# Kernel tuning notes

Hardware: AMD Instinct MI355X
Metric: run time of the kernel (lower is better)

The kernel has to match this reference:

```python
import jax, jax.numpy as jnp
import numpy as np

H = 1024  # hidden_size
O = 768   # output_size == g_bert_emb_dim
B = 256   # batch
T = 256   # tgt_len
SRC_LEN = 2


def setup_inputs() -> dict:
    key = jax.random.key(0)
    ks = jax.random.split(key, 9)
    s = 1.0 / np.sqrt(H)
    return {
        "src": jax.random.normal(ks[0], (SRC_LEN, B, O), jnp.float32),
        "tgt": jax.random.randint(ks[1], (T, B), 0, 30000),
        "hidden": jax.random.normal(ks[2], (1, B, H), jnp.float32),
        # PyTorch nn.GRU params, gate order (r, z, n)
        "w_ih": jax.random.uniform(ks[3], (3 * H, O), jnp.float32, -s, s),
        "w_hh": jax.random.uniform(ks[4], (3 * H, H), jnp.float32, -s, s),
        "b_ih": jax.random.uniform(ks[5], (3 * H,), jnp.float32, -s, s),
        "b_hh": jax.random.uniform(ks[6], (3 * H,), jnp.float32, -s, s),
        # nn.Linear(hidden_size, output_size)
        "w_fc": jax.random.uniform(ks[7], (O, H), jnp.float32, -s, s),
        "b_fc": jax.random.uniform(ks[8], (O,), jnp.float32, -s, s),
    }


def reference(src, tgt, hidden, w_ih, w_hh, b_ih, b_hh, w_fc, b_fc):
    tgt_len = tgt.shape[0]

    def step(carry, _):
        x, h = carry  # x: [B, O] (previous fc output), h: [B, H]
        gi = x @ w_ih.T + b_ih          # [B, 3H]
        gh = h @ w_hh.T + b_hh          # [B, 3H]
        i_r, i_z, i_n = jnp.split(gi, 3, axis=-1)
        h_r, h_z, h_n = jnp.split(gh, 3, axis=-1)
        r = jax.nn.sigmoid(i_r + h_r)
        z = jax.nn.sigmoid(i_z + h_z)
        n = jnp.tanh(i_n + r * h_n)
        h_new = (1.0 - z) * n + z * h
        y = h_new @ w_fc.T + b_fc       # fc feedback, [B, O]
        return (y, h_new), y

    x0 = src[0]          # [B, O]
    h0 = hidden[0]       # [B, H] (num_layers = 1)
    _, outputs = jax.lax.scan(step, (x0, h0), None, length=tgt_len)
    return outputs  # [T, B, O]
```

## Files before the change

kernel.cpp:

```cpp
#include <hip/hip_runtime.h>
#include <stdint.h>

#define HDIM 1024
#define ODIM 768
#define BDIM 256
#define TLEN 256
#define G3 (3*HDIM)

typedef __attribute__((ext_vector_type(4))) float f32x4;
typedef __attribute__((ext_vector_type(8))) short s16x8;
typedef __attribute__((ext_vector_type(2))) unsigned long long u64x2;

#define SENT64 0xFFFFFFFFFFFFFFFFull

static __device__ __forceinline__ unsigned short f2bf(float f) {
  uint32_t u = __builtin_bit_cast(uint32_t, f);
  return (unsigned short)((u + 0x7fffu + ((u >> 16) & 1u)) >> 16);
}


__global__ void k_f32_to_bf16(const float* __restrict__ in, unsigned short* __restrict__ out, int n4) {
  int i = blockIdx.x * 256 + threadIdx.x;
  if (i >= n4) return;
  float4 v = ((const float4*)in)[i];
  ushort4 o;
  o.x = f2bf(v.x); o.y = f2bf(v.y); o.z = f2bf(v.z); o.w = f2bf(v.w);
  ((ushort4*)out)[i] = o;
}

__global__ void k_transpose_f32_bf16(const float* __restrict__ in, unsigned short* __restrict__ out, int R, int C) {
  __shared__ float tile[32][33];
  int c0 = blockIdx.x * 32, r0 = blockIdx.y * 32;
  int tx = threadIdx.x, ty = threadIdx.y;
  #pragma unroll
  for (int i = 0; i < 32; i += 8)
    tile[ty + i][tx] = in[(size_t)(r0 + ty + i) * C + (c0 + tx)];
  __syncthreads();
  #pragma unroll
  for (int i = 0; i < 32; i += 8)
    out[(size_t)(c0 + ty + i) * R + (r0 + tx)] = f2bf(tile[tx][ty + i]);
}

__global__ void k_bcomb(const float* __restrict__ w_ih, const float* __restrict__ b_ih,
                        const float* __restrict__ b_fc, float* __restrict__ bc) {
  int gw = (blockIdx.x * 256 + threadIdx.x) >> 6;
  int lane = threadIdx.x & 63;
  if (gw >= G3) return;
  const float* row = w_ih + (size_t)gw * ODIM;
  float s = 0.f;
  for (int o = lane; o < ODIM; o += 64) s += row[o] * b_fc[o];
  #pragma unroll
  for (int off = 32; off; off >>= 1) s += __shfl_down(s, off);
  if (lane == 0) bc[gw] = s + b_ih[gw];
}

template<bool OUT_BF16, bool ADD_BIAS>
__global__ __launch_bounds__(256) void k_gemm_bt(
    const unsigned short* __restrict__ A,
    const unsigned short* __restrict__ Bm,
    const float* __restrict__ bias,
    void* __restrict__ Cout,
    int M, int N, int K)
{
  __shared__ f32x4 red[4][32][64];
  int m0 = blockIdx.x * 64, n0 = blockIdx.y * 128;
  int w = threadIdx.x >> 6, lane = threadIdx.x & 63;
  int c = lane & 15, klane = (lane >> 4) << 3;
  int kpw = K >> 2, kw0 = w * kpw;
  f32x4 acc[4][8];
  #pragma unroll
  for (int mf = 0; mf < 4; mf++)
    #pragma unroll
    for (int nf = 0; nf < 8; nf++) acc[mf][nf] = f32x4{0.f, 0.f, 0.f, 0.f};

  for (int kk = 0; kk < kpw; kk += 32) {
    int kb = kw0 + kk + klane;
    s16x8 a[4], b[8];
    #pragma unroll
    for (int mf = 0; mf < 4; mf++)
      a[mf] = *(const s16x8*)(A + (size_t)(m0 + mf*16 + c) * K + kb);
    #pragma unroll
    for (int nf = 0; nf < 8; nf++)
      b[nf] = *(const s16x8*)(Bm + (size_t)(n0 + nf*16 + c) * K + kb);
    #pragma unroll
    for (int mf = 0; mf < 4; mf++)
      #pragma unroll
      for (int nf = 0; nf < 8; nf++)
        acc[mf][nf] = __builtin_amdgcn_mfma_f32_16x16x32_bf16(a[mf], b[nf], acc[mf][nf], 0, 0, 0);
  }
  #pragma unroll
  for (int mf = 0; mf < 4; mf++)
    #pragma unroll
    for (int nf = 0; nf < 8; nf++)
      red[w][mf*8+nf][lane] = acc[mf][nf];
  __syncthreads();
  #pragma unroll
  for (int nf = 0; nf < 8; nf++) {
    f32x4 s = red[0][w*8+nf][lane];
    #pragma unroll
    for (int w2 = 1; w2 < 4; w2++) s += red[w2][w*8+nf][lane];
    int col = n0 + nf*16 + c;
    float bv = 0.f;
    if constexpr (ADD_BIAS) bv = bias[col];
    int rb = m0 + w*16 + ((lane >> 4) << 2);
    #pragma unroll
    for (int i = 0; i < 4; i++) {
      float val = s[i] + bv;
      if constexpr (OUT_BF16)
        ((unsigned short*)Cout)[(size_t)(rb + i) * N + col] = f2bf(val);
      else
        ((float*)Cout)[(size_t)(rb + i) * N + col] = val;
    }
  }
}

__global__ __launch_bounds__(256) void k_gemm_hseq(
    const unsigned long long* __restrict__ Ahx,
    const unsigned short* __restrict__ Bm,
    const float* __restrict__ bias,
    float* __restrict__ Cout)
{
  const int M = TLEN*BDIM, N = ODIM, K = HDIM;
  __shared__ f32x4 red[4][32][64];
  int m0 = blockIdx.x * 64, n0 = blockIdx.y * 128;
  int w = threadIdx.x >> 6, lane = threadIdx.x & 63;
  int c = lane & 15, klane = (lane >> 4) << 3;
  int kpw = K >> 2, kw0 = w * kpw;
  const int tb = m0 >> 8, mgb = (m0 >> 6) & 3;
  f32x4 acc[4][8];
  #pragma unroll
  for (int mf = 0; mf < 4; mf++)
    #pragma unroll
    for (int nf = 0; nf < 8; nf++) acc[mf][nf] = f32x4{0.f, 0.f, 0.f, 0.f};

  for (int kk = 0; kk < kpw; kk += 32) {
    int kb = kw0 + kk + klane;
    int uk = kb >> 2;
    s16x8 a[4], b[8];
    #pragma unroll
    for (int mf = 0; mf < 4; mf++)
      a[mf] = *(const s16x8*)(Ahx + (((size_t)((tb*64 + (uk>>2))*4 + mgb)) << 8)
                                   + (size_t)(mf*16 + c)*4 + (uk & 3));
    #pragma unroll
    for (int nf = 0; nf < 8; nf++)
      b[nf] = *(const s16x8*)(Bm + (size_t)(n0 + nf*16 + c) * K + kb);
    #pragma unroll
    for (int mf = 0; mf < 4; mf++)
      #pragma unroll
      for (int nf = 0; nf < 8; nf++)
        acc[mf][nf] = __builtin_amdgcn_mfma_f32_16x16x32_bf16(a[mf], b[nf], acc[mf][nf], 0, 0, 0);
  }
  #pragma unroll
  for (int mf = 0; mf < 4; mf++)
    #pragma unroll
    for (int nf = 0; nf < 8; nf++)
      red[w][mf*8+nf][lane] = acc[mf][nf];
  __syncthreads();
  #pragma unroll
  for (int nf = 0; nf < 8; nf++) {
    f32x4 s = red[0][w*8+nf][lane];
    #pragma unroll
    for (int w2 = 1; w2 < 4; w2++) s += red[w2][w*8+nf][lane];
    int col = n0 + nf*16 + c;
    float bv = bias[col];
    int rb = m0 + w*16 + ((lane >> 4) << 2);
    #pragma unroll
    for (int i = 0; i < 4; i++)
      Cout[(size_t)(rb + i) * N + col] = s[i] + bv;
  }
}

__global__ __launch_bounds__(256, 1) void k_gru_persist(
    const unsigned short* __restrict__ h0b,
    const unsigned short* __restrict__ wcomb,
    const unsigned short* __restrict__ whh,
    const float* __restrict__ bcomb,
    const float* __restrict__ bhh,
    const float* __restrict__ gi0,
    const float* __restrict__ hidden0,
    unsigned long long* __restrict__ hx64)
{
  __shared__ f32x4 red[4][24][64];
  __shared__ unsigned long long tile64[64][4];
  unsigned short* tile = (unsigned short*)tile64;

  const int wg = blockIdx.x;
  const int mg = wg & 3, p = wg >> 2;
  const int tid = threadIdx.x;
  const int w = tid >> 6, lane = tid & 63;
  const int c = lane & 15, klane = (lane >> 4) << 3, rq = (lane >> 4) << 2;
  const int u0 = p * 16, u = u0 + c, m0 = mg * 64;
  const int wk0 = w * 256;
  const int rp = lane >> 5;
  const int q0 = ((lane >> 4) & 1) << 1;
  const int cprod = 16 * w + (lane & 15);

  const float bcr = bcomb[u], bcz = bcomb[HDIM + u], bcn = bcomb[2*HDIM + u];
  const float bhr = bhh[u],   bhz = bhh[HDIM + u],   bhn = bhh[2*HDIM + u];

  s16x8 wr[6][8];
  #pragma unroll
  for (int g = 0; g < 6; g++) {
    const unsigned short* W = (g < 3) ? (wcomb + (size_t)g * HDIM * HDIM)
                                      : (whh   + (size_t)(g - 3) * HDIM * HDIM);
    const unsigned short* Wrow = W + (size_t)(u0 + c) * HDIM + wk0 + klane;
    #pragma unroll
    for (int ks = 0; ks < 8; ks++)
      wr[g][ks] = *(const s16x8*)(Wrow + ks * 32);
  }

  float hcar[4];

  #pragma unroll 1
  for (int t = 0; t < TLEN; t++) {
    s16x8 a[8][4];
    if (t == 0) {
      #pragma unroll
      for (int ks = 0; ks < 8; ks++)
        #pragma unroll
        for (int mf = 0; mf < 4; mf++)
          a[ks][mf] = *(const s16x8*)(h0b + (size_t)(m0 + mf*16 + c) * HDIM + wk0 + ks*32 + klane);
    } else {
      unsigned long long* hxp = hx64 + (size_t)(t - 1) * (64*4*256);
      {
        const unsigned long long* cn = hxp + (((size_t)(cprod*4 + mg)) << 8) + 255;
        for (;;) {
          unsigned long long v = __hip_atomic_load(cn, __ATOMIC_RELAXED, __HIP_MEMORY_SCOPE_AGENT);
          if (__all(v != SENT64)) break;
          __builtin_amdgcn_s_sleep(1);
        }
      }
      u64x2 va[8][4];
      #pragma unroll
      for (int ks = 0; ks < 8; ks++)
        #pragma unroll
        for (int mf = 0; mf < 4; mf++)
          va[ks][mf] = *(const u64x2*)(hxp + (((size_t)((16*w + 2*ks + rp)*4 + mg)) << 8)
                                            + (size_t)(mf*16 + c)*4 + q0);
      unsigned int bad = 0;
      #pragma unroll
      for (int ks = 0; ks < 8; ks++)
        #pragma unroll
        for (int mf = 0; mf < 4; mf++)
          bad |= (unsigned int)(va[ks][mf][0] == SENT64) | (unsigned int)(va[ks][mf][1] == SENT64);
      if (__any((int)bad)) {
        #pragma unroll
        for (int ks = 0; ks < 8; ks++)
          #pragma unroll
          for (int mf = 0; mf < 4; mf++) {
            unsigned long long* pb = hxp + (((size_t)((16*w + 2*ks + rp)*4 + mg)) << 8)
                                         + (size_t)(mf*16 + c)*4 + q0;
            #pragma unroll
            for (int hh = 0; hh < 2; hh++) {
              if (va[ks][mf][hh] == SENT64) {
                unsigned long long v;
                do {
                  v = __hip_atomic_load(pb + hh, __ATOMIC_RELAXED, __HIP_MEMORY_SCOPE_AGENT);
                } while (v == SENT64);
                pb[hh] = v;
                va[ks][mf][hh] = v;
              }
            }
          }
      }
      #pragma unroll
      for (int ks = 0; ks < 8; ks++)
        #pragma unroll
        for (int mf = 0; mf < 4; mf++)
          a[ks][mf] = __builtin_bit_cast(s16x8, va[ks][mf]);
    }

    f32x4 acc[4][6];
    #pragma unroll
    for (int mf = 0; mf < 4; mf++)
      #pragma unroll
      for (int g = 0; g < 6; g++) acc[mf][g] = f32x4{0.f, 0.f, 0.f, 0.f};
    #pragma unroll
    for (int ks = 0; ks < 8; ks++)
      #pragma unroll
      for (int g = 0; g < 6; g++)
        #pragma unroll
        for (int mf = 0; mf < 4; mf++)
          acc[mf][g] = __builtin_amdgcn_mfma_f32_16x16x32_bf16(a[ks][mf], wr[g][ks], acc[mf][g], 0, 0, 0);

    #pragma unroll
    for (int mf = 0; mf < 4; mf++) {
      if (mf != w) {
        #pragma unroll
        for (int g = 0; g < 6; g++) red[w][mf*6 + g][lane] = acc[mf][g];
      }
    }
    f32x4 s[6];
    #pragma unroll
    for (int mf = 0; mf < 4; mf++) {
      if (mf == w) {
        #pragma unroll
        for (int g = 0; g < 6; g++) s[g] = acc[mf][g];
      }
    }
    __syncthreads();
    #pragma unroll
    for (int w2 = 0; w2 < 4; w2++) {
      if (w2 != w) {
        #pragma unroll
        for (int g = 0; g < 6; g++) s[g] += red[w2][w*6 + g][lane];
      }
    }
    __syncthreads();

    const int rbl = w*16 + rq;
    #pragma unroll
    for (int i = 0; i < 4; i++) {
      int r = m0 + rbl + i;
      float gir, giz, gin;
      if (t == 0) {
        gir = gi0[(size_t)r * G3 + u];
        giz = gi0[(size_t)r * G3 + HDIM + u];
        gin = gi0[(size_t)r * G3 + 2*HDIM + u];
        hcar[i] = hidden0[(size_t)r * HDIM + u];
      } else {
        gir = s[0][i] + bcr; giz = s[1][i] + bcz; gin = s[2][i] + bcn;
      }
      float ghr = s[3][i] + bhr, ghz = s[4][i] + bhz, ghn = s[5][i] + bhn;
      float rg = 1.f / (1.f + __expf(-(gir + ghr)));
      float zg = 1.f / (1.f + __expf(-(giz + ghz)));
      float pn = gin + rg * ghn;
      pn = fminf(fmaxf(pn, -15.f), 15.f);
      float e2 = __expf(2.f * pn);
      float ng = (e2 - 1.f) / (e2 + 1.f);
      float hv = (1.f - zg) * ng + zg * hcar[i];
      hcar[i] = hv;
      tile[(rbl + i) * 16 + c] = f2bf(hv);
    }

    {
      unsigned long long v = tile64[tid >> 2][tid & 3];
      unsigned long long* dst = hx64 + (size_t)t * (64*4*256)
                              + (((size_t)(p*4 + mg)) << 8) + tid;
      __hip_atomic_store(dst, v, __ATOMIC_RELAXED, __HIP_MEMORY_SCOPE_AGENT);
    }
  }
}

__global__ __launch_bounds__(256) void k_gru_step(
    const unsigned short* __restrict__ A1, int K1,
    const unsigned short* __restrict__ W1,
    const float* __restrict__ b1,
    const unsigned short* __restrict__ A2,
    const unsigned short* __restrict__ W2,
    const float* __restrict__ b2,
    const float* __restrict__ hprev,
    float* __restrict__ hout,
    unsigned short* __restrict__ hseq,
    int fused)
{
  __shared__ f32x4 red[4][24][64];
  int ublk = blockIdx.x & 63, mg = blockIdx.x >> 6;
  int u0 = ublk * 16, m0 = mg * 64;
  int w = threadIdx.x >> 6, lane = threadIdx.x & 63;
  int c = lane & 15, klane = (lane >> 4) << 3;
  f32x4 acc[6][4];
  #pragma unroll
  for (int g = 0; g < 6; g++)
    #pragma unroll
    for (int mf = 0; mf < 4; mf++) acc[g][mf] = f32x4{0.f, 0.f, 0.f, 0.f};

  if (fused) {
    const int kpw = HDIM >> 2;
    int kw0 = w * kpw;
    for (int kk = 0; kk < kpw; kk += 32) {
      int kb = kw0 + kk + klane;
      s16x8 a[4], bg[6];
      #pragma unroll
      for (int mf = 0; mf < 4; mf++)
        a[mf] = *(const s16x8*)(A2 + (size_t)(m0 + mf*16 + c) * HDIM + kb);
      #pragma unroll
      for (int g = 0; g < 3; g++) {
        bg[g]   = *(const s16x8*)(W1 + (size_t)(g*HDIM + u0 + c) * HDIM + kb);
        bg[g+3] = *(const s16x8*)(W2 + (size_t)(g*HDIM + u0 + c) * HDIM + kb);
      }
      #pragma unroll
      for (int g = 0; g < 6; g++)
        #pragma unroll
        for (int mf = 0; mf < 4; mf++)
          acc[g][mf] = __builtin_amdgcn_mfma_f32_16x16x32_bf16(a[mf], bg[g], acc[g][mf], 0, 0, 0);
    }
  } else {
    {
      int kpw = K1 >> 2, kw0 = w * kpw;
      for (int kk = 0; kk < kpw; kk += 32) {
        int kb = kw0 + kk + klane;
        s16x8 a[4], bg[3];
        #pragma unroll
        for (int mf = 0; mf < 4; mf++)
          a[mf] = *(const s16x8*)(A1 + (size_t)(m0 + mf*16 + c) * K1 + kb);
        #pragma unroll
        for (int g = 0; g < 3; g++)
          bg[g] = *(const s16x8*)(W1 + (size_t)(g*HDIM + u0 + c) * K1 + kb);
        #pragma unroll
        for (int g = 0; g < 3; g++)
          #pragma unroll
          for (int mf = 0; mf < 4; mf++)
            acc[g][mf] = __builtin_amdgcn_mfma_f32_16x16x32_bf16(a[mf], bg[g], acc[g][mf], 0, 0, 0);
      }
    }
    {
      int kpw = HDIM >> 2, kw0 = w * kpw;
      for (int kk = 0; kk < kpw; kk += 32) {
        int kb = kw0 + kk + klane;
        s16x8 a[4], bg[3];
        #pragma unroll
        for (int mf = 0; mf < 4; mf++)
          a[mf] = *(const s16x8*)(A2 + (size_t)(m0 + mf*16 + c) * HDIM + kb);
        #pragma unroll
        for (int g = 0; g < 3; g++)
          bg[g] = *(const s16x8*)(W2 + (size_t)(g*HDIM + u0 + c) * HDIM + kb);
        #pragma unroll
        for (int g = 0; g < 3; g++)
          #pragma unroll
          for (int mf = 0; mf < 4; mf++)
            acc[g+3][mf] = __builtin_amdgcn_mfma_f32_16x16x32_bf16(a[mf], bg[g], acc[g+3][mf], 0, 0, 0);
      }
    }
  }

  #pragma unroll
  for (int g = 0; g < 6; g++)
    #pragma unroll
    for (int mf = 0; mf < 4; mf++)
      red[w][g*4+mf][lane] = acc[g][mf];
  __syncthreads();

  f32x4 gg[6];
  #pragma unroll
  for (int g = 0; g < 6; g++) {
    f32x4 sum = red[0][g*4+w][lane];
    #pragma unroll
    for (int w2 = 1; w2 < 4; w2++) sum += red[w2][g*4+w][lane];
    gg[g] = sum;
  }
  int u = u0 + c;
  float b1r = b1[u], b1z = b1[HDIM+u], b1n = b1[2*HDIM+u];
  float b2r = b2[u], b2z = b2[HDIM+u], b2n = b2[2*HDIM+u];
  int rb = m0 + w*16 + ((lane >> 4) << 2);
  #pragma unroll
  for (int i = 0; i < 4; i++) {
    float pre_r = gg[0][i] + b1r + gg[3][i] + b2r;
    float pre_z = gg[1][i] + b1z + gg[4][i] + b2z;
    float ghn  = gg[5][i] + b2n;
    float r = 1.f / (1.f + __expf(-pre_r));
    float z = 1.f / (1.f + __expf(-pre_z));
    float pn = gg[2][i] + b1n + r * ghn;
    pn = fminf(fmaxf(pn, -15.f), 15.f);
    float e2 = __expf(2.f * pn);
    float n = (e2 - 1.f) / (e2 + 1.f);
    size_t idx = (size_t)(rb + i) * HDIM + u;
    float hp = hprev[idx];
    float hn = (1.f - z) * n + z * hp;
    hout[idx] = hn;
    hseq[idx] = f2bf(hn);
  }
}


extern "C" void kernel_launch(void* const* d_in, const int* in_sizes, int n_in,
                              void* d_out, int out_size, void* d_ws, size_t ws_size,
                              hipStream_t stream) {
  const float* src    = (const float*)d_in[0];
  const float* hidden = (const float*)d_in[2];
  const float* w_ih   = (const float*)d_in[3];
  const float* w_hh   = (const float*)d_in[4];
  const float* b_ih   = (const float*)d_in[5];
  const float* b_hh   = (const float*)d_in[6];
  const float* w_fc   = (const float*)d_in[7];
  const float* b_fc   = (const float*)d_in[8];
  float* out = (float*)d_out;

  uint8_t* ws = (uint8_t*)d_ws;
  size_t off = 0;
  auto alloc = [&](size_t bytes) -> void* {
    void* pp = ws + off;
    off += (bytes + 255) & ~(size_t)255;
    return pp;
  };
  unsigned short* wih_b  = (unsigned short*)alloc((size_t)G3*ODIM*2);
  unsigned short* whh_b  = (unsigned short*)alloc((size_t)G3*HDIM*2);
  unsigned short* wfc_b  = (unsigned short*)alloc((size_t)ODIM*HDIM*2);
  unsigned short* wfcT_b = (unsigned short*)alloc((size_t)HDIM*ODIM*2);
  unsigned short* wcomb  = (unsigned short*)alloc((size_t)G3*HDIM*2);
  unsigned short* src0_b = (unsigned short*)alloc((size_t)BDIM*ODIM*2);
  unsigned short* h0_b   = (unsigned short*)alloc((size_t)BDIM*HDIM*2);
  float* bcomb = (float*)alloc((size_t)G3*4);
  float* hbuf0 = (float*)alloc((size_t)BDIM*HDIM*4);
  float* hbuf1 = (float*)alloc((size_t)BDIM*HDIM*4);
  unsigned short* hpp = (unsigned short*)alloc((size_t)2*BDIM*HDIM*2);
  unsigned short* hseq = (unsigned short*)alloc((size_t)TLEN*BDIM*HDIM*2);
  float* gi0 = (float*)alloc((size_t)BDIM*G3*4);
  bool big = (off <= ws_size);

  k_f32_to_bf16<<<G3*ODIM/4/256, 256, 0, stream>>>(w_ih, wih_b, G3*ODIM/4);
  k_f32_to_bf16<<<G3*HDIM/4/256, 256, 0, stream>>>(w_hh, whh_b, G3*HDIM/4);
  k_f32_to_bf16<<<ODIM*HDIM/4/256, 256, 0, stream>>>(w_fc, wfc_b, ODIM*HDIM/4);
  k_f32_to_bf16<<<BDIM*ODIM/4/256, 256, 0, stream>>>(src, src0_b, BDIM*ODIM/4);
  k_f32_to_bf16<<<BDIM*HDIM/4/256, 256, 0, stream>>>(hidden, h0_b, BDIM*HDIM/4);
  k_transpose_f32_bf16<<<dim3(HDIM/32, ODIM/32), dim3(32, 8), 0, stream>>>(w_fc, wfcT_b, ODIM, HDIM);
  k_gemm_bt<true, false><<<dim3(G3/64, HDIM/128), 256, 0, stream>>>(wih_b, wfcT_b, nullptr, wcomb, G3, HDIM, ODIM);
  k_bcomb<<<G3/4, 256, 0, stream>>>(w_ih, b_ih, b_fc, bcomb);

  if (big) {
    hipMemsetAsync(hseq, 0xFF, (size_t)TLEN*BDIM*HDIM*2, stream);
    k_gemm_bt<false, true><<<dim3(BDIM/64, G3/128), 256, 0, stream>>>(
        src0_b, wih_b, b_ih, gi0, BDIM, G3, ODIM);
    k_gru_persist<<<256, 256, 0, stream>>>(h0_b, wcomb, whh_b, bcomb, b_hh,
                                           gi0, hidden,
                                           (unsigned long long*)hseq);
    k_gemm_hseq<<<dim3(TLEN*BDIM/64, ODIM/128), 256, 0, stream>>>(
        (const unsigned long long*)hseq, wfc_b, b_fc, out);
  } else {
    for (int t = 0; t < TLEN; t++) {
      const unsigned short* aprev = (t == 0) ? h0_b : hpp + (size_t)((t-1)&1)*BDIM*HDIM;
      unsigned short* hs_cur = hpp + (size_t)(t&1)*BDIM*HDIM;
      const float* hprev_f = (t == 0) ? hidden : ((t & 1) ? hbuf0 : hbuf1);
      float* hout_f = (t & 1) ? hbuf1 : hbuf0;
      if (t == 0) {
        k_gru_step<<<256, 256, 0, stream>>>(src0_b, ODIM, wih_b, b_ih,
            aprev, whh_b, b_hh, hprev_f, hout_f, hs_cur, 0);
      } else {
        k_gru_step<<<256, 256, 0, stream>>>(aprev, HDIM, wcomb, bcomb,
            aprev, whh_b, b_hh, hprev_f, hout_f, hs_cur, 1);
      }
      k_gemm_bt<false, true><<<dim3(BDIM/64, ODIM/128), 256, 0, stream>>>(
          hs_cur, wfc_b, b_fc, out + (size_t)t*BDIM*ODIM, BDIM, ODIM, HDIM);
    }
  }
}
```

Measured before the change: 2.209 ms.

## Split persistent GRU gate GEMMs across two wave groups with 512 threads

The persistent GRU kernel now runs 512 threads per block. Waves 0-3 compute the three input-side gates from wcomb and waves 4-7 compute the three hidden-side gates from whh, so each wave holds half the weight registers and issues half the MFMAs per step. The per-step hidden-state fragments are loaded and MFMA'd in two halves to limit live registers. Shared-memory reductions are split into two buffers, and the output tile row stride is padded to avoid bank conflicts. In exchange, both wave groups read the same hidden-state fragments, and only half the waves do the elementwise gate math and stores.

```diff
diff --git a/kernel.cpp b/kernel.cpp
--- a/kernel.cpp
+++ b/kernel.cpp
@@ -120,7 +120,7 @@
     const float* __restrict__ bias,
     float* __restrict__ Cout)
 {
-  const int M = TLEN*BDIM, N = ODIM, K = HDIM;
+  const int N = ODIM, K = HDIM;
   __shared__ f32x4 red[4][32][64];
   int m0 = blockIdx.x * 64, n0 = blockIdx.y * 128;
   int w = threadIdx.x >> 6, lane = threadIdx.x & 63;
@@ -170,7 +170,7 @@
   }
 }
 
-__global__ __launch_bounds__(256, 1) void k_gru_persist(
+__global__ __launch_bounds__(512) void k_gru_persist(
     const unsigned short* __restrict__ h0b,
     const unsigned short* __restrict__ wcomb,
     const unsigned short* __restrict__ whh,
@@ -180,30 +180,31 @@
     const float* __restrict__ hidden0,
     unsigned long long* __restrict__ hx64)
 {
-  __shared__ f32x4 red[4][24][64];
-  __shared__ unsigned long long tile64[64][4];
+  __shared__ f32x4 redA[4][12][64];
+  __shared__ f32x4 redB[4][12][64];
+  __shared__ unsigned long long tile64[64][5];
   unsigned short* tile = (unsigned short*)tile64;
 
   const int wg = blockIdx.x;
   const int mg = wg & 3, p = wg >> 2;
   const int tid = threadIdx.x;
-  const int w = tid >> 6, lane = tid & 63;
+  const int wv = tid >> 6, lane = tid & 63;
+  const int kw = wv & 3, gg = wv >> 2;
   const int c = lane & 15, klane = (lane >> 4) << 3, rq = (lane >> 4) << 2;
   const int u0 = p * 16, u = u0 + c, m0 = mg * 64;
-  const int wk0 = w * 256;
+  const int wk0 = kw * 256;
   const int rp = lane >> 5;
   const int q0 = ((lane >> 4) & 1) << 1;
-  const int cprod = 16 * w + (lane & 15);
+  const int cprod = 16 * kw + (lane & 15);
 
   const float bcr = bcomb[u], bcz = bcomb[HDIM + u], bcn = bcomb[2*HDIM + u];
   const float bhr = bhh[u],   bhz = bhh[HDIM + u],   bhn = bhh[2*HDIM + u];
 
-  s16x8 wr[6][8];
-  #pragma unroll
-  for (int g = 0; g < 6; g++) {
-    const unsigned short* W = (g < 3) ? (wcomb + (size_t)g * HDIM * HDIM)
-                                      : (whh   + (size_t)(g - 3) * HDIM * HDIM);
-    const unsigned short* Wrow = W + (size_t)(u0 + c) * HDIM + wk0 + klane;
+  const unsigned short* Wbase = gg ? whh : wcomb;
+  s16x8 wr[3][8];
+  #pragma unroll
+  for (int g = 0; g < 3; g++) {
+    const unsigned short* Wrow = Wbase + (size_t)(g * HDIM + u0 + c) * HDIM + wk0 + klane;
     #pragma unroll
     for (int ks = 0; ks < 8; ks++)
       wr[g][ks] = *(const s16x8*)(Wrow + ks * 32);
@@ -213,13 +214,30 @@
 
   #pragma unroll 1
   for (int t = 0; t < TLEN; t++) {
-    s16x8 a[8][4];
+    f32x4 acc[4][3];
+    #pragma unroll
+    for (int mf = 0; mf < 4; mf++)
+      #pragma unroll
+      for (int g = 0; g < 3; g++) acc[mf][g] = f32x4{0.f, 0.f, 0.f, 0.f};
+
     if (t == 0) {
       #pragma unroll
-      for (int ks = 0; ks < 8; ks++)
-        #pragma unroll
-        for (int mf = 0; mf < 4; mf++)
-          a[ks][mf] = *(const s16x8*)(h0b + (size_t)(m0 + mf*16 + c) * HDIM + wk0 + ks*32 + klane);
+      for (int pp = 0; pp < 2; pp++) {
+        s16x8 a[4][4];
+        #pragma unroll
+        for (int ks = 0; ks < 4; ks++)
+          #pragma unroll
+          for (int mf = 0; mf < 4; mf++)
+            a[ks][mf] = *(const s16x8*)(h0b + (size_t)(m0 + mf*16 + c) * HDIM
+                                             + wk0 + (pp*4 + ks)*32 + klane);
+        #pragma unroll
+        for (int ks = 0; ks < 4; ks++)
+          #pragma unroll
+          for (int g = 0; g < 3; g++)
+            #pragma unroll
+            for (int mf = 0; mf < 4; mf++)
+              acc[mf][g] = __builtin_amdgcn_mfma_f32_16x16x32_bf16(a[ks][mf], wr[g][ks? (pp*4+ks) : pp*4], acc[mf][g], 0, 0, 0);
+      }
     } else {
       unsigned long long* hxp = hx64 + (size_t)(t - 1) * (64*4*256);
       {
@@ -230,114 +248,123 @@
           __builtin_amdgcn_s_sleep(1);
         }
       }
-      u64x2 va[8][4];
-      #pragma unroll
-      for (int ks = 0; ks < 8; ks++)
-        #pragma unroll
-        for (int mf = 0; mf < 4; mf++)
-          va[ks][mf] = *(const u64x2*)(hxp + (((size_t)((16*w + 2*ks + rp)*4 + mg)) << 8)
-                                            + (size_t)(mf*16 + c)*4 + q0);
-      unsigned int bad = 0;
-      #pragma unroll
-      for (int ks = 0; ks < 8; ks++)
-        #pragma unroll
-        for (int mf = 0; mf < 4; mf++)
-          bad |= (unsigned int)(va[ks][mf][0] == SENT64) | (unsigned int)(va[ks][mf][1] == SENT64);
-      if (__any((int)bad)) {
-        #pragma unroll
-        for (int ks = 0; ks < 8; ks++)
-          #pragma unroll
-          for (int mf = 0; mf < 4; mf++) {
-            unsigned long long* pb = hxp + (((size_t)((16*w + 2*ks + rp)*4 + mg)) << 8)
-                                         + (size_t)(mf*16 + c)*4 + q0;
+      #pragma unroll
+      for (int pp = 0; pp < 2; pp++) {
+        u64x2 va[4][4];
+        #pragma unroll
+        for (int ks = 0; ks < 4; ks++)
+          #pragma unroll
+          for (int mf = 0; mf < 4; mf++)
+            va[ks][mf] = *(const u64x2*)(hxp
+                + (((size_t)((16*kw + 2*(pp*4 + ks) + rp)*4 + mg)) << 8)
+                + (size_t)(mf*16 + c)*4 + q0);
+        unsigned int bad = 0;
+        #pragma unroll
+        for (int ks = 0; ks < 4; ks++)
+          #pragma unroll
+          for (int mf = 0; mf < 4; mf++)
+            bad |= (unsigned int)(va[ks][mf][0] == SENT64) | (unsigned int)(va[ks][mf][1] == SENT64);
+        if (__any((int)bad)) {
+          #pragma unroll
+          for (int ks = 0; ks < 4; ks++)
             #pragma unroll
-            for (int hh = 0; hh < 2; hh++) {
-              if (va[ks][mf][hh] == SENT64) {
-                unsigned long long v;
-                do {
-                  v = __hip_atomic_load(pb + hh, __ATOMIC_RELAXED, __HIP_MEMORY_SCOPE_AGENT);
-                } while (v == SENT64);
-                pb[hh] = v;
-                va[ks][mf][hh] = v;
+            for (int mf = 0; mf < 4; mf++) {
+              unsigned long long* pb = hxp
+                  + (((size_t)((16*kw + 2*(pp*4 + ks) + rp)*4 + mg)) << 8)
+                  + (size_t)(mf*16 + c)*4 + q0;
+              #pragma unroll
+              for (int hh = 0; hh < 2; hh++) {
+                if (va[ks][mf][hh] == SENT64) {
+                  unsigned long long v;
+                  do {
+                    v = __hip_atomic_load(pb + hh, __ATOMIC_RELAXED, __HIP_MEMORY_SCOPE_AGENT);
+                  } while (v == SENT64);
+                  pb[hh] = v;
+                  va[ks][mf][hh] = v;
+                }
               }
             }
-          }
-      }
-      #pragma unroll
-      for (int ks = 0; ks < 8; ks++)
-        #pragma unroll
-        for (int mf = 0; mf < 4; mf++)
-          a[ks][mf] = __builtin_bit_cast(s16x8, va[ks][mf]);
-    }
-
-    f32x4 acc[4][6];
-    #pragma unroll
-    for (int mf = 0; mf < 4; mf++)
-      #pragma unroll
-      for (int g = 0; g < 6; g++) acc[mf][g] = f32x4{0.f, 0.f, 0.f, 0.f};
-    #pragma unroll
-    for (int ks = 0; ks < 8; ks++)
-      #pragma unroll
-      for (int g = 0; g < 6; g++)
-        #pragma unroll
-        for (int mf = 0; mf < 4; mf++)
-          acc[mf][g] = __builtin_amdgcn_mfma_f32_16x16x32_bf16(a[ks][mf], wr[g][ks], acc[mf][g], 0, 0, 0);
-
-    #pragma unroll
-    for (int mf = 0; mf < 4; mf++) {
-      if (mf != w) {
-        #pragma unroll
-        for (int g = 0; g < 6; g++) red[w][mf*6 + g][lane] = acc[mf][g];
-      }
-    }
-    f32x4 s[6];
-    #pragma unroll
-    for (int mf = 0; mf < 4; mf++) {
-      if (mf == w) {
-        #pragma unroll
-        for (int g = 0; g < 6; g++) s[g] = acc[mf][g];
-      }
+        }
+        #pragma unroll
+        for (int ks = 0; ks < 4; ks++)
+          #pragma unroll
+          for (int g = 0; g < 3; g++)
+            #pragma unroll
+            for (int mf = 0; mf < 4; mf++)
+              acc[mf][g] = __builtin_amdgcn_mfma_f32_16x16x32_bf16(
+                  __builtin_bit_cast(s16x8, va[ks][mf]), wr[g][pp*4 + ks], acc[mf][g], 0, 0, 0);
+      }
+    }
+
+    f32x4 sc[3], sh[3];
+    if (gg == 0) {
+      #pragma unroll
+      for (int mf = 0; mf < 4; mf++) {
+        if (mf != kw) {
+          #pragma unroll
+          for (int g = 0; g < 3; g++) redA[kw][mf*3 + g][lane] = acc[mf][g];
+        } else {
+          #pragma unroll
+          for (int g = 0; g < 3; g++) sc[g] = acc[mf][g];
+        }
+      }
+    } else {
+      #pragma unroll
+      for (int mf = 0; mf < 4; mf++)
+        #pragma unroll
+        for (int g = 0; g < 3; g++) redB[kw][mf*3 + g][lane] = acc[mf][g];
     }
     __syncthreads();
-    #pragma unroll
-    for (int w2 = 0; w2 < 4; w2++) {
-      if (w2 != w) {
-        #pragma unroll
-        for (int g = 0; g < 6; g++) s[g] += red[w2][w*6 + g][lane];
-      }
+    if (gg == 0) {
+      #pragma unroll
+      for (int k2 = 0; k2 < 4; k2++) {
+        if (k2 != kw) {
+          #pragma unroll
+          for (int g = 0; g < 3; g++) sc[g] += redA[k2][kw*3 + g][lane];
+        }
+      }
+      #pragma unroll
+      for (int g = 0; g < 3; g++) sh[g] = redB[0][kw*3 + g][lane];
+      #pragma unroll
+      for (int k2 = 1; k2 < 4; k2++)
+        #pragma unroll
+        for (int g = 0; g < 3; g++) sh[g] += redB[k2][kw*3 + g][lane];
     }
     __syncthreads();
 
-    const int rbl = w*16 + rq;
-    #pragma unroll
-    for (int i = 0; i < 4; i++) {
-      int r = m0 + rbl + i;
-      float gir, giz, gin;
-      if (t == 0) {
-        gir = gi0[(size_t)r * G3 + u];
-        giz = gi0[(size_t)r * G3 + HDIM + u];
-        gin = gi0[(size_t)r * G3 + 2*HDIM + u];
-        hcar[i] = hidden0[(size_t)r * HDIM + u];
-      } else {
-        gir = s[0][i] + bcr; giz = s[1][i] + bcz; gin = s[2][i] + bcn;
-      }
-      float ghr = s[3][i] + bhr, ghz = s[4][i] + bhz, ghn = s[5][i] + bhn;
-      float rg = 1.f / (1.f + __expf(-(gir + ghr)));
-      float zg = 1.f / (1.f + __expf(-(giz + ghz)));
-      float pn = gin + rg * ghn;
-      pn = fminf(fmaxf(pn, -15.f), 15.f);
-      float e2 = __expf(2.f * pn);
-      float ng = (e2 - 1.f) / (e2 + 1.f);
-      float hv = (1.f - zg) * ng + zg * hcar[i];
-      hcar[i] = hv;
-      tile[(rbl + i) * 16 + c] = f2bf(hv);
-    }
-
-    {
-      unsigned long long v = tile64[tid >> 2][tid & 3];
-      unsigned long long* dst = hx64 + (size_t)t * (64*4*256)
-                              + (((size_t)(p*4 + mg)) << 8) + tid;
-      __hip_atomic_store(dst, v, __ATOMIC_RELAXED, __HIP_MEMORY_SCOPE_AGENT);
+    if (gg == 0) {
+      const int rbl = kw*16 + rq;
+      #pragma unroll
+      for (int i = 0; i < 4; i++) {
+        int r = m0 + rbl + i;
+        float gir, giz, gin;
+        if (t == 0) {
+          gir = gi0[(size_t)r * G3 + u];
+          giz = gi0[(size_t)r * G3 + HDIM + u];
+          gin = gi0[(size_t)r * G3 + 2*HDIM + u];
+          hcar[i] = hidden0[(size_t)r * HDIM + u];
+        } else {
+          gir = sc[0][i] + bcr; giz = sc[1][i] + bcz; gin = sc[2][i] + bcn;
+        }
+        float ghr = sh[0][i] + bhr, ghz = sh[1][i] + bhz, ghn = sh[2][i] + bhn;
+        float rg = 1.f / (1.f + __expf(-(gir + ghr)));
+        float zg = 1.f / (1.f + __expf(-(giz + ghz)));
+        float pn = gin + rg * ghn;
+        pn = fminf(fmaxf(pn, -15.f), 15.f);
+        float e2 = __expf(2.f * pn);
+        float ng = (e2 - 1.f) / (e2 + 1.f);
+        float hv = (1.f - zg) * ng + zg * hcar[i];
+        hcar[i] = hv;
+        tile[(rbl + i) * 20 + c] = f2bf(hv);
+      }
+
+      {
+        int row = kw*16 + (lane >> 2), pq = lane & 3;
+        unsigned long long v = tile64[row][pq];
+        unsigned long long* dst = hx64 + (size_t)t * (64*4*256)
+                                + (((size_t)(p*4 + mg)) << 8) + (kw*64 + lane);
+        __hip_atomic_store(dst, v, __ATOMIC_RELAXED, __HIP_MEMORY_SCOPE_AGENT);
+      }
     }
   }
 }
@@ -511,7 +538,7 @@
     hipMemsetAsync(hseq, 0xFF, (size_t)TLEN*BDIM*HDIM*2, stream);
     k_gemm_bt<false, true><<<dim3(BDIM/64, G3/128), 256, 0, stream>>>(
         src0_b, wih_b, b_ih, gi0, BDIM, G3, ODIM);
-    k_gru_persist<<<256, 256, 0, stream>>>(h0_b, wcomb, whh_b, bcomb, b_hh,
+    k_gru_persist<<<256, 512, 0, stream>>>(h0_b, wcomb, whh_b, bcomb, b_hh,
                                            gi0, hidden,
                                            (unsigned long long*)hseq);
     k_gemm_hseq<<<dim3(TLEN*BDIM/64, ODIM/128), 256, 0, stream>>>(
```

New measurement: 2.367 ms. 1.07x slower.

## Fuse fc output projection into persistent GRU kernel, drop separate hseq GEMM

Applied to the files above, without the earlier changes.

The separate post-loop GEMM that projected all hidden states through w_fc is removed. Instead, 192 of the 256 persistent workgroups compute the fc output for the previous step's hidden state, reusing the already-loaded A fragments, and write y directly. A tail section waits for the last hidden state and computes the final step's output. This removes a large standalone GEMM and the re-read of hseq, but adds extra MFMA work and w_fc loads inside the latency-critical recurrent loop, unevenly across workgroups.

```diff
diff --git a/kernel.cpp b/kernel.cpp
--- a/kernel.cpp
+++ b/kernel.cpp
@@ -114,62 +114,6 @@
   }
 }
 
-__global__ __launch_bounds__(256) void k_gemm_hseq(
-    const unsigned long long* __restrict__ Ahx,
-    const unsigned short* __restrict__ Bm,
-    const float* __restrict__ bias,
-    float* __restrict__ Cout)
-{
-  const int M = TLEN*BDIM, N = ODIM, K = HDIM;
-  __shared__ f32x4 red[4][32][64];
-  int m0 = blockIdx.x * 64, n0 = blockIdx.y * 128;
-  int w = threadIdx.x >> 6, lane = threadIdx.x & 63;
-  int c = lane & 15, klane = (lane >> 4) << 3;
-  int kpw = K >> 2, kw0 = w * kpw;
-  const int tb = m0 >> 8, mgb = (m0 >> 6) & 3;
-  f32x4 acc[4][8];
-  #pragma unroll
-  for (int mf = 0; mf < 4; mf++)
-    #pragma unroll
-    for (int nf = 0; nf < 8; nf++) acc[mf][nf] = f32x4{0.f, 0.f, 0.f, 0.f};
-
-  for (int kk = 0; kk < kpw; kk += 32) {
-    int kb = kw0 + kk + klane;
-    int uk = kb >> 2;
-    s16x8 a[4], b[8];
-    #pragma unroll
-    for (int mf = 0; mf < 4; mf++)
-      a[mf] = *(const s16x8*)(Ahx + (((size_t)((tb*64 + (uk>>2))*4 + mgb)) << 8)
-                                   + (size_t)(mf*16 + c)*4 + (uk & 3));
-    #pragma unroll
-    for (int nf = 0; nf < 8; nf++)
-      b[nf] = *(const s16x8*)(Bm + (size_t)(n0 + nf*16 + c) * K + kb);
-    #pragma unroll
-    for (int mf = 0; mf < 4; mf++)
-      #pragma unroll
-      for (int nf = 0; nf < 8; nf++)
-        acc[mf][nf] = __builtin_amdgcn_mfma_f32_16x16x32_bf16(a[mf], b[nf], acc[mf][nf], 0, 0, 0);
-  }
-  #pragma unroll
-  for (int mf = 0; mf < 4; mf++)
-    #pragma unroll
-    for (int nf = 0; nf < 8; nf++)
-      red[w][mf*8+nf][lane] = acc[mf][nf];
-  __syncthreads();
-  #pragma unroll
-  for (int nf = 0; nf < 8; nf++) {
-    f32x4 s = red[0][w*8+nf][lane];
-    #pragma unroll
-    for (int w2 = 1; w2 < 4; w2++) s += red[w2][w*8+nf][lane];
-    int col = n0 + nf*16 + c;
-    float bv = bias[col];
-    int rb = m0 + w*16 + ((lane >> 4) << 2);
-    #pragma unroll
-    for (int i = 0; i < 4; i++)
-      Cout[(size_t)(rb + i) * N + col] = s[i] + bv;
-  }
-}
-
 __global__ __launch_bounds__(256, 1) void k_gru_persist(
     const unsigned short* __restrict__ h0b,
     const unsigned short* __restrict__ wcomb,
@@ -178,9 +122,13 @@
     const float* __restrict__ bhh,
     const float* __restrict__ gi0,
     const float* __restrict__ hidden0,
+    const unsigned short* __restrict__ wfc,
+    const float* __restrict__ bfc,
+    float* __restrict__ yout,
     unsigned long long* __restrict__ hx64)
 {
   __shared__ f32x4 red[4][24][64];
+  __shared__ f32x4 redY[4][4][64];
   __shared__ unsigned long long tile64[64][4];
   unsigned short* tile = (unsigned short*)tile64;
 
@@ -194,6 +142,11 @@
   const int rp = lane >> 5;
   const int q0 = ((lane >> 4) & 1) << 1;
   const int cprod = 16 * w + (lane & 15);
+  const int rbl = w*16 + rq;
+
+  const bool doy = (p < 48);
+  const float ybias = doy ? bfc[p*16 + c] : 0.f;
+  const unsigned short* wfrow = wfc + (size_t)(p*16 + c) * HDIM + wk0 + klane;
 
   const float bcr = bcomb[u], bcz = bcomb[HDIM + u], bcn = bcomb[2*HDIM + u];
   const float bhr = bhh[u],   bhz = bhh[HDIM + u],   bhn = bhh[2*HDIM + u];
@@ -283,6 +236,19 @@
         for (int mf = 0; mf < 4; mf++)
           acc[mf][g] = __builtin_amdgcn_mfma_f32_16x16x32_bf16(a[ks][mf], wr[g][ks], acc[mf][g], 0, 0, 0);
 
+    f32x4 yacc[4];
+    if (doy && t > 0) {
+      #pragma unroll
+      for (int mf = 0; mf < 4; mf++) yacc[mf] = f32x4{0.f, 0.f, 0.f, 0.f};
+      #pragma unroll
+      for (int ks = 0; ks < 8; ks++) {
+        s16x8 wf = *(const s16x8*)(wfrow + ks * 32);
+        #pragma unroll
+        for (int mf = 0; mf < 4; mf++)
+          yacc[mf] = __builtin_amdgcn_mfma_f32_16x16x32_bf16(a[ks][mf], wf, yacc[mf], 0, 0, 0);
+      }
+    }
+
     #pragma unroll
     for (int mf = 0; mf < 4; mf++) {
       if (mf != w) {
@@ -290,6 +256,11 @@
         for (int g = 0; g < 6; g++) red[w][mf*6 + g][lane] = acc[mf][g];
       }
     }
+    if (doy && t > 0) {
+      #pragma unroll
+      for (int mf = 0; mf < 4; mf++)
+        if (mf != w) redY[w][mf][lane] = yacc[mf];
+    }
     f32x4 s[6];
     #pragma unroll
     for (int mf = 0; mf < 4; mf++) {
@@ -306,9 +277,15 @@
         for (int g = 0; g < 6; g++) s[g] += red[w2][w*6 + g][lane];
       }
     }
+    f32x4 ysum;
+    if (doy && t > 0) {
+      ysum = yacc[w];
+      #pragma unroll
+      for (int w2 = 0; w2 < 4; w2++)
+        if (w2 != w) ysum += redY[w2][w][lane];
+    }
     __syncthreads();
 
-    const int rbl = w*16 + rq;
     #pragma unroll
     for (int i = 0; i < 4; i++) {
       int r = m0 + rbl + i;
@@ -338,6 +315,83 @@
       unsigned long long* dst = hx64 + (size_t)t * (64*4*256)
                               + (((size_t)(p*4 + mg)) << 8) + tid;
       __hip_atomic_store(dst, v, __ATOMIC_RELAXED, __HIP_MEMORY_SCOPE_AGENT);
+    }
+
+    if (doy && t > 0) {
+      #pragma unroll
+      for (int i = 0; i < 4; i++) {
+        int r = m0 + rbl + i;
+        yout[((size_t)(t - 1) * BDIM + r) * ODIM + p*16 + c] = ysum[i] + ybias;
+      }
+    }
+  }
+
+  if (doy) {
+    unsigned long long* hxp = hx64 + (size_t)(TLEN - 1) * (64*4*256);
+    {
+      const unsigned long long* cn = hxp + (((size_t)(cprod*4 + mg)) << 8) + 255;
+      for (;;) {
+        unsigned long long v = __hip_atomic_load(cn, __ATOMIC_RELAXED, __HIP_MEMORY_SCOPE_AGENT);
+        if (__all(v != SENT64)) break;
+        __builtin_amdgcn_s_sleep(1);
+      }
+    }
+    u64x2 va[8][4];
+    #pragma unroll
+    for (int ks = 0; ks < 8; ks++)
+      #pragma unroll
+      for (int mf = 0; mf < 4; mf++)
+        va[ks][mf] = *(const u64x2*)(hxp + (((size_t)((16*w + 2*ks + rp)*4 + mg)) << 8)
+                                          + (size_t)(mf*16 + c)*4 + q0);
+    unsigned int bad = 0;
+    #pragma unroll
+    for (int ks = 0; ks < 8; ks++)
+      #pragma unroll
+      for (int mf = 0; mf < 4; mf++)
+        bad |= (unsigned int)(va[ks][mf][0] == SENT64) | (unsigned int)(va[ks][mf][1] == SENT64);
+    if (__any((int)bad)) {
+      #pragma unroll
+      for (int ks = 0; ks < 8; ks++)
+        #pragma unroll
+        for (int mf = 0; mf < 4; mf++) {
+          unsigned long long* pb = hxp + (((size_t)((16*w + 2*ks + rp)*4 + mg)) << 8)
+                                       + (size_t)(mf*16 + c)*4 + q0;
+          #pragma unroll
+          for (int hh = 0; hh < 2; hh++) {
+            if (va[ks][mf][hh] == SENT64) {
+              unsigned long long v;
+              do {
+                v = __hip_atomic_load(pb + hh, __ATOMIC_RELAXED, __HIP_MEMORY_SCOPE_AGENT);
+              } while (v == SENT64);
+              pb[hh] = v;
+              va[ks][mf][hh] = v;
+            }
+          }
+        }
+    }
+    f32x4 yacc[4];
+    #pragma unroll
+    for (int mf = 0; mf < 4; mf++) yacc[mf] = f32x4{0.f, 0.f, 0.f, 0.f};
+    #pragma unroll
+    for (int ks = 0; ks < 8; ks++) {
+      s16x8 wf = *(const s16x8*)(wfrow + ks * 32);
+      #pragma unroll
+      for (int mf = 0; mf < 4; mf++)
+        yacc[mf] = __builtin_amdgcn_mfma_f32_16x16x32_bf16(
+            __builtin_bit_cast(s16x8, va[ks][mf]), wf, yacc[mf], 0, 0, 0);
+    }
+    #pragma unroll
+    for (int mf = 0; mf < 4; mf++)
+      if (mf != w) redY[w][mf][lane] = yacc[mf];
+    __syncthreads();
+    f32x4 ysum = yacc[w];
+    #pragma unroll
+    for (int w2 = 0; w2 < 4; w2++)
+      if (w2 != w) ysum += redY[w2][w][lane];
+    #pragma unroll
+    for (int i = 0; i < 4; i++) {
+      int r = m0 + rbl + i;
+      yout[((size_t)(TLEN - 1) * BDIM + r) * ODIM + p*16 + c] = ysum[i] + ybias;
     }
   }
 }
@@ -512,10 +566,8 @@
     k_gemm_bt<false, true><<<dim3(BDIM/64, G3/128), 256, 0, stream>>>(
         src0_b, wih_b, b_ih, gi0, BDIM, G3, ODIM);
     k_gru_persist<<<256, 256, 0, stream>>>(h0_b, wcomb, whh_b, bcomb, b_hh,
-                                           gi0, hidden,
+                                           gi0, hidden, wfc_b, b_fc, out,
                                            (unsigned long long*)hseq);
-    k_gemm_hseq<<<dim3(TLEN*BDIM/64, ODIM/128), 256, 0, stream>>>(
-        (const unsigned long long*)hseq, wfc_b, b_fc, out);
   } else {
     for (int t = 0; t < TLEN; t++) {
       const unsigned short* aprev = (t == 0) ? h0_b : hpp + (size_t)((t-1)&1)*BDIM*HDIM;
```

New measurement: 4.123 ms. 86.6% more time.
